# Kernel optimization log

Hardware: AMD Instinct MI355X
Metric: run time of the kernel (lower is better)

Reference implementation:

```python
import jax, jax.numpy as jnp
import numpy as np

B, CIN, COUT, K, E, H, W = 32, 128, 256, 3, 8, 64, 64


def setup_inputs() -> dict:
    key = jax.random.key(0)
    k1, k2, k3, k4 = jax.random.split(key, 4)
    x = jax.random.normal(k1, (B, CIN, H, W), dtype=jnp.float32)
    expert_weight = jax.random.normal(k2, (E, COUT, CIN, K, K), dtype=jnp.float32)
    # nn.Linear(in_channels, num_experts): weight [E, CIN], bias [E]
    bound = 1.0 / np.sqrt(CIN)
    routing_w = jax.random.uniform(k3, (E, CIN), minval=-bound, maxval=bound, dtype=jnp.float32)
    routing_b = jax.random.uniform(k4, (E,), minval=-bound, maxval=bound, dtype=jnp.float32)
    return {"x": x, "expert_weight": expert_weight, "routing_w": routing_w, "routing_b": routing_b}


def reference(x, expert_weight, routing_w, routing_b):
    # routing: global-avg-pool -> linear -> softmax over experts
    pooled = x.mean(axis=(2, 3))                             # [B, CIN]
    logits = pooled @ routing_w.T + routing_b                # [B, E]
    rweights = jax.nn.softmax(logits, axis=-1)               # [B, E]
    # per-sample combined conv weights: [B, COUT, CIN, K, K]
    cw = jnp.einsum('be,eoikl->boikl', rweights, expert_weight)

    def conv_one(xi, wi):
        # xi: [CIN, H, W], wi: [COUT, CIN, K, K]; VALID conv, stride 1
        return jax.lax.conv_general_dilated(
            xi[None], wi, window_strides=(1, 1), padding='VALID',
            dimension_numbers=('NCHW', 'OIHW', 'NCHW'))[0]

    return jax.vmap(conv_one)(x, cw)                         # [B, COUT, H-K+1, W-K+1]
```

## Files before the change

### kernel.cpp

```cpp
#include <hip/hip_runtime.h>
#include <hip/hip_bf16.h>


#define CC_B    32
#define CC_CIN  128
#define CC_COUT 256
#define CC_NP   3844
#define CC_NT   18

typedef __attribute__((ext_vector_type(8))) short bf16x8;
typedef __attribute__((ext_vector_type(4))) float f32x4;

__global__ void cc_nhwc(const float* __restrict__ x, __hip_bfloat16* __restrict__ xn,
                        float* __restrict__ psum) {
    const int b = blockIdx.x >> 6, y = blockIdx.x & 63;
    __shared__ float lds[64 * 129];
    __shared__ float sred[256];
    const int t = threadIdx.x;
    const float* src = x + (size_t)b * CC_CIN * 4096 + y * 64;
#pragma unroll
    for (int i = 0; i < 32; ++i) {
        const int idx = i * 256 + t;
        const int cin = idx >> 6, xx = idx & 63;
        lds[xx * 129 + cin] = src[(size_t)cin * 4096 + xx];
    }
    __syncthreads();
    __hip_bfloat16* dst = xn + ((size_t)b * 4096 + y * 64) * CC_CIN;
#pragma unroll
    for (int j = 0; j < 4; ++j) {
        const int cidx = j * 256 + t;
        const int xx = cidx >> 4, c8 = (cidx & 15) * 8;
        union { __hip_bfloat16 h[8]; uint4 v; } u;
#pragma unroll
        for (int jj = 0; jj < 8; ++jj) u.h[jj] = __float2bfloat16(lds[xx * 129 + c8 + jj]);
        *reinterpret_cast<uint4*>(dst + (size_t)xx * CC_CIN + c8) = u.v;
    }
    const int cin = t & 127, xh = (t >> 7) * 32;
    float s = 0.f;
#pragma unroll
    for (int xx = 0; xx < 32; ++xx) s += lds[(xh + xx) * 129 + cin];
    sred[t] = s;
    __syncthreads();
    if (t < 128) psum[((size_t)b * 64 + y) * CC_CIN + t] = sred[t] + sred[t + 128];
}

__global__ void cc_route(const float* __restrict__ psum,
                         const float* __restrict__ rw_w,
                         const float* __restrict__ rw_b,
                         float* __restrict__ rweights) {
    const int b = blockIdx.x, c = threadIdx.x;
    __shared__ float pl[128];
    __shared__ float lg[8];
    const float* p = psum + (size_t)b * 64 * CC_CIN + c;
    float s = 0.f;
#pragma unroll 8
    for (int y = 0; y < 64; ++y) s += p[(size_t)y * CC_CIN];
    pl[c] = s * (1.f / 4096.f);
    __syncthreads();
    if (c < 8) {
        const float* w = rw_w + c * CC_CIN;
        float a = rw_b[c];
#pragma unroll 8
        for (int i = 0; i < CC_CIN; ++i) a += pl[i] * w[i];
        lg[c] = a;
    }
    __syncthreads();
    if (c == 0) {
        float m = lg[0];
#pragma unroll
        for (int e = 1; e < 8; ++e) m = fmaxf(m, lg[e]);
        float ex[8], sm = 0.f;
#pragma unroll
        for (int e = 0; e < 8; ++e) { ex[e] = __expf(lg[e] - m); sm += ex[e]; }
#pragma unroll
        for (int e = 0; e < 8; ++e) rweights[b * 8 + e] = ex[e] / sm;
    }
}

__global__ void cc_combine(const float* __restrict__ ew,
                           const float* __restrict__ rw,
                           __hip_bfloat16* __restrict__ cw) {
    const int t9 = blockIdx.x >> 8;
    const int cout = blockIdx.x & 255;
    const int cin = threadIdx.x;
    __shared__ float rws[256];
    rws[cin] = rw[cin];
    rws[cin + 128] = rw[cin + 128];
    __syncthreads();
    float wv[8];
    const size_t base = ((size_t)cout * CC_CIN + cin) * 9 + t9;
#pragma unroll
    for (int e = 0; e < 8; ++e) wv[e] = ew[base + (size_t)e * (CC_COUT * CC_CIN * 9)];
#pragma unroll 4
    for (int b = 0; b < CC_B; ++b) {
        float acc = 0.f;
#pragma unroll
        for (int e = 0; e < 8; ++e) acc += rws[b * 8 + e] * wv[e];
        cw[(((size_t)b * 9 + t9) * CC_COUT + cout) * CC_CIN + cin] = __float2bfloat16(acc);
    }
}

__device__ __forceinline__ void gload_lds16(const void* g, void* l) {
    __builtin_amdgcn_global_load_lds(
        (const __attribute__((address_space(1))) unsigned int*)g,
        (__attribute__((address_space(3))) unsigned int*)l, 16, 0, 0);
}

__global__ __launch_bounds__(256, 2) void cc_conv(
    const __hip_bfloat16* __restrict__ xn,
    const __hip_bfloat16* __restrict__ cw,
    float* __restrict__ out)
{
    __shared__ __align__(16) char smem[73728];
    const int l   = blockIdx.x;
    const int xcd = l & 7, li = l >> 3;
    const int b   = 4 * xcd + li / 42;
    const int r2  = li % 42;
    const int nt  = r2 >> 1, mt = r2 & 1;
    const int m0  = mt * 128;
    const int n0  = nt * 186;
    const int y0  = 3 * nt;

    const int tid = threadIdx.x;
    const int wid = tid >> 6, lane = tid & 63;
    const int waveM = wid >> 1, waveN = wid & 1;

    f32x4 acc[4][6];
#pragma unroll
    for (int i = 0; i < 4; ++i)
#pragma unroll
        for (int j = 0; j < 6; ++j) acc[i][j] = (f32x4){0.f, 0.f, 0.f, 0.f};

    const int gsw = (lane & 7) ^ (lane >> 3);
    const __hip_bfloat16* cwb = cw + (size_t)b * 9 * CC_COUT * CC_CIN;
    const __hip_bfloat16* xnb = xn + (size_t)b * 4096 * CC_CIN;

    int laOff[4];
#pragma unroll
    for (int i = 0; i < 4; ++i) {
        const int row = wid * 32 + i * 8 + (lane >> 3);
        laOff[i] = (m0 + row) * CC_CIN + gsw * 8;
    }
    auto stageA = [&](int t) {
        const int h = t / 9, t9 = t - 9 * h;
        const int aoff = t9 * (CC_COUT * CC_CIN) + h * 64;
        char* Ab = smem + (t & 1) * 16384 + wid * 4096;
#pragma unroll
        for (int i = 0; i < 4; ++i)
            gload_lds16(cwb + aoff + laOff[i], Ab + i * 1024);
    };

    char* Bres = smem + 32768;
    auto stageB = [&](int h) {
#pragma unroll
        for (int i = 0; i < 10; ++i) {
            const int row = i * 32 + wid * 8 + (lane >> 3);
            const int yy = row >> 6, x = row & 63;
            int yin = y0 + yy; if (yin > 63) yin = 63;
            gload_lds16(xnb + ((size_t)yin * 64 + x) * CC_CIN + h * 64 + gsw * 8,
                        Bres + i * 4096 + wid * 1024);
        }
    };

    const int rl = lane & 15, q = lane >> 4;

    int pixB[6];
#pragma unroll
    for (int nf = 0; nf < 6; ++nf) {
        int c = waveN * 96 + nf * 16 + rl;
        if (c > 185) c = 185;
        int p = n0 + c; if (p > CC_NP - 1) p = CC_NP - 1;
        const int oy = p / 62;
        pixB[nf] = (oy - y0) * 64 + (p - 62 * oy);
    }

    stageB(0);
    stageA(0);
    stageA(1);

#pragma unroll
    for (int t = 0; t < CC_NT; ++t) {
        const int h = t / 9, t9 = t - 9 * h;
        const int kyx = (t9 / 3) * 64 + (t9 - 3 * (t9 / 3));
        const char* Ab = smem + (t & 1) * 16384;

        if (t < CC_NT - 1) asm volatile("s_waitcnt vmcnt(4)" ::: "memory");
        else               asm volatile("s_waitcnt vmcnt(0)" ::: "memory");
        asm volatile("s_barrier" ::: "memory");

        bf16x8 af[8], bf[12];
#pragma unroll
        for (int mf = 0; mf < 4; ++mf) {
            const int r = waveM * 64 + mf * 16 + rl;
            const char* ap = Ab + r * 128;
            af[mf * 2 + 0] = *(const bf16x8*)(ap + (((q) ^ (r & 7)) * 16));
            af[mf * 2 + 1] = *(const bf16x8*)(ap + (((4 + q) ^ (r & 7)) * 16));
        }
#pragma unroll
        for (int nf = 0; nf < 6; ++nf) {
            const int row = pixB[nf] + kyx;
            const char* bp = Bres + row * 128;
            bf[nf * 2 + 0] = *(const bf16x8*)(bp + (((q) ^ (row & 7)) * 16));
            bf[nf * 2 + 1] = *(const bf16x8*)(bp + (((4 + q) ^ (row & 7)) * 16));
        }
        __builtin_amdgcn_s_setprio(1);
#pragma unroll
        for (int kk = 0; kk < 2; ++kk)
#pragma unroll
            for (int mf = 0; mf < 4; ++mf)
#pragma unroll
                for (int nf = 0; nf < 6; ++nf)
                    acc[mf][nf] = __builtin_amdgcn_mfma_f32_16x16x32_bf16(
                        af[mf * 2 + kk], bf[nf * 2 + kk], acc[mf][nf], 0, 0, 0);
        __builtin_amdgcn_s_setprio(0);

        asm volatile("s_waitcnt lgkmcnt(0)" ::: "memory");
        asm volatile("s_barrier" ::: "memory");
        if (t == 8) stageB(1);
        if (t + 2 < CC_NT) stageA(t + 2);
    }

    const int q4 = (lane >> 4) * 4;
#pragma unroll
    for (int mf = 0; mf < 4; ++mf) {
        const int crow = m0 + waveM * 64 + mf * 16 + q4;
#pragma unroll
        for (int nf = 0; nf < 6; ++nf) {
            const int c = waveN * 96 + nf * 16 + (lane & 15);
            const int p = n0 + c;
            if (c < 186 && p < CC_NP) {
                const size_t ob = ((size_t)b * CC_COUT + crow) * CC_NP + p;
#pragma unroll
                for (int j = 0; j < 4; ++j) out[ob + (size_t)j * CC_NP] = acc[mf][nf][j];
            }
        }
    }
}

extern "C" void kernel_launch(void* const* d_in, const int* in_sizes, int n_in,
                              void* d_out, int out_size, void* d_ws, size_t ws_size,
                              hipStream_t stream) {
    const float* x   = (const float*)d_in[0];
    const float* ew  = (const float*)d_in[1];
    const float* rww = (const float*)d_in[2];
    const float* rwb = (const float*)d_in[3];
    float* out = (float*)d_out;
    char* ws = (char*)d_ws;

    __hip_bfloat16* xnhwc = (__hip_bfloat16*)ws;
    __hip_bfloat16* cwcmb = (__hip_bfloat16*)(ws + 33554432);
    float* psum   = (float*)(ws + 52428800);
    float* rwts   = (float*)(ws + 53493760);

    cc_nhwc<<<dim3(CC_B * 64), dim3(256), 0, stream>>>(x, xnhwc, psum);
    cc_route<<<dim3(CC_B), dim3(128), 0, stream>>>(psum, rww, rwb, rwts);
    cc_combine<<<dim3(9 * CC_COUT), dim3(128), 0, stream>>>(ew, rwts, cwcmb);
    cc_conv<<<dim3(1344), dim3(256), 0, stream>>>(xnhwc, cwcmb, out);
}
```

Baseline: 141.2 us.

## Switch conv GEMM to 32x32x16 MFMA with two-row pixel tiles

The implicit-GEMM conv now uses 32x32x16 bf16 MFMA instructions in place of 16x16x32, with 2x2 fragments per wave. Each block covers 2 output rows (124 pixels) instead of 3 rows (186 pixels), which removes padding waste and the clamping logic and raises the grid from 1344 to 1984 blocks. The larger MFMA is meant to cut LDS fragment reads per FLOP, and the smaller tile is meant to improve load balance. In exchange, the B tile reuse per block drops, and the occupancy hint of 2 blocks per CU is removed from the launch bounds.

```diff
diff --git a/kernel.cpp b/kernel.cpp
--- a/kernel.cpp
+++ b/kernel.cpp
@@ -9,7 +9,7 @@
 #define CC_NT   18
 
 typedef __attribute__((ext_vector_type(8))) short bf16x8;
-typedef __attribute__((ext_vector_type(4))) float f32x4;
+typedef __attribute__((ext_vector_type(16))) float f32x16;
 
 __global__ void cc_nhwc(const float* __restrict__ x, __hip_bfloat16* __restrict__ xn,
                         float* __restrict__ psum) {
@@ -106,30 +106,32 @@
         (__attribute__((address_space(3))) unsigned int*)l, 16, 0, 0);
 }
 
-__global__ __launch_bounds__(256, 2) void cc_conv(
+__global__ __launch_bounds__(256) void cc_conv(
     const __hip_bfloat16* __restrict__ xn,
     const __hip_bfloat16* __restrict__ cw,
     float* __restrict__ out)
 {
-    __shared__ __align__(16) char smem[73728];
+    __shared__ __align__(16) char smem[65536];
     const int l   = blockIdx.x;
     const int xcd = l & 7, li = l >> 3;
-    const int b   = 4 * xcd + li / 42;
-    const int r2  = li % 42;
+    const int b   = 4 * xcd + li / 62;
+    const int r2  = li % 62;
     const int nt  = r2 >> 1, mt = r2 & 1;
     const int m0  = mt * 128;
-    const int n0  = nt * 186;
-    const int y0  = 3 * nt;
+    const int n0  = nt * 124;
+    const int y0  = 2 * nt;
 
     const int tid = threadIdx.x;
     const int wid = tid >> 6, lane = tid & 63;
     const int waveM = wid >> 1, waveN = wid & 1;
 
-    f32x4 acc[4][6];
-#pragma unroll
-    for (int i = 0; i < 4; ++i)
-#pragma unroll
-        for (int j = 0; j < 6; ++j) acc[i][j] = (f32x4){0.f, 0.f, 0.f, 0.f};
+    f32x16 acc[2][2];
+#pragma unroll
+    for (int i = 0; i < 2; ++i)
+#pragma unroll
+        for (int j = 0; j < 2; ++j)
+#pragma unroll
+            for (int v = 0; v < 16; ++v) acc[i][j][v] = 0.f;
 
     const int gsw = (lane & 7) ^ (lane >> 3);
     const __hip_bfloat16* cwb = cw + (size_t)b * 9 * CC_COUT * CC_CIN;
@@ -153,25 +155,22 @@
     char* Bres = smem + 32768;
     auto stageB = [&](int h) {
 #pragma unroll
-        for (int i = 0; i < 10; ++i) {
+        for (int i = 0; i < 8; ++i) {
             const int row = i * 32 + wid * 8 + (lane >> 3);
             const int yy = row >> 6, x = row & 63;
-            int yin = y0 + yy; if (yin > 63) yin = 63;
-            gload_lds16(xnb + ((size_t)yin * 64 + x) * CC_CIN + h * 64 + gsw * 8,
+            gload_lds16(xnb + ((size_t)(y0 + yy) * 64 + x) * CC_CIN + h * 64 + gsw * 8,
                         Bres + i * 4096 + wid * 1024);
         }
     };
 
-    const int rl = lane & 15, q = lane >> 4;
-
-    int pixB[6];
-#pragma unroll
-    for (int nf = 0; nf < 6; ++nf) {
-        int c = waveN * 96 + nf * 16 + rl;
-        if (c > 185) c = 185;
-        int p = n0 + c; if (p > CC_NP - 1) p = CC_NP - 1;
-        const int oy = p / 62;
-        pixB[nf] = (oy - y0) * 64 + (p - 62 * oy);
+    const int l31 = lane & 31, q2 = lane >> 5;
+
+    int pixB[2];
+#pragma unroll
+    for (int nf = 0; nf < 2; ++nf) {
+        int c = nf * 32 + l31;
+        if (c > 61) c = 61;
+        pixB[nf] = waveN * 64 + c;
     }
 
     stageB(0);
@@ -188,30 +187,29 @@
         else               asm volatile("s_waitcnt vmcnt(0)" ::: "memory");
         asm volatile("s_barrier" ::: "memory");
 
-        bf16x8 af[8], bf[12];
-#pragma unroll
-        for (int mf = 0; mf < 4; ++mf) {
-            const int r = waveM * 64 + mf * 16 + rl;
-            const char* ap = Ab + r * 128;
-            af[mf * 2 + 0] = *(const bf16x8*)(ap + (((q) ^ (r & 7)) * 16));
-            af[mf * 2 + 1] = *(const bf16x8*)(ap + (((4 + q) ^ (r & 7)) * 16));
-        }
-#pragma unroll
-        for (int nf = 0; nf < 6; ++nf) {
-            const int row = pixB[nf] + kyx;
-            const char* bp = Bres + row * 128;
-            bf[nf * 2 + 0] = *(const bf16x8*)(bp + (((q) ^ (row & 7)) * 16));
-            bf[nf * 2 + 1] = *(const bf16x8*)(bp + (((4 + q) ^ (row & 7)) * 16));
+        bf16x8 af[2][4], bf[2][4];
+#pragma unroll
+        for (int ks = 0; ks < 4; ++ks) {
+#pragma unroll
+            for (int mf = 0; mf < 2; ++mf) {
+                const int r = waveM * 64 + mf * 32 + l31;
+                af[mf][ks] = *(const bf16x8*)(Ab + r * 128 + (((ks * 2 + q2) ^ (r & 7)) * 16));
+            }
+#pragma unroll
+            for (int nf = 0; nf < 2; ++nf) {
+                const int row = pixB[nf] + kyx;
+                bf[nf][ks] = *(const bf16x8*)(Bres + row * 128 + (((ks * 2 + q2) ^ (row & 7)) * 16));
+            }
         }
         __builtin_amdgcn_s_setprio(1);
 #pragma unroll
-        for (int kk = 0; kk < 2; ++kk)
-#pragma unroll
-            for (int mf = 0; mf < 4; ++mf)
-#pragma unroll
-                for (int nf = 0; nf < 6; ++nf)
-                    acc[mf][nf] = __builtin_amdgcn_mfma_f32_16x16x32_bf16(
-                        af[mf * 2 + kk], bf[nf * 2 + kk], acc[mf][nf], 0, 0, 0);
+        for (int ks = 0; ks < 4; ++ks)
+#pragma unroll
+            for (int mf = 0; mf < 2; ++mf)
+#pragma unroll
+                for (int nf = 0; nf < 2; ++nf)
+                    acc[mf][nf] = __builtin_amdgcn_mfma_f32_32x32x16_bf16(
+                        af[mf][ks], bf[nf][ks], acc[mf][nf], 0, 0, 0);
         __builtin_amdgcn_s_setprio(0);
 
         asm volatile("s_waitcnt lgkmcnt(0)" ::: "memory");
@@ -220,18 +218,21 @@
         if (t + 2 < CC_NT) stageA(t + 2);
     }
 
-    const int q4 = (lane >> 4) * 4;
-#pragma unroll
-    for (int mf = 0; mf < 4; ++mf) {
-        const int crow = m0 + waveM * 64 + mf * 16 + q4;
-#pragma unroll
-        for (int nf = 0; nf < 6; ++nf) {
-            const int c = waveN * 96 + nf * 16 + (lane & 15);
-            const int p = n0 + c;
-            if (c < 186 && p < CC_NP) {
-                const size_t ob = ((size_t)b * CC_COUT + crow) * CC_NP + p;
-#pragma unroll
-                for (int j = 0; j < 4; ++j) out[ob + (size_t)j * CC_NP] = acc[mf][nf][j];
+#pragma unroll
+    for (int mf = 0; mf < 2; ++mf) {
+#pragma unroll
+        for (int nf = 0; nf < 2; ++nf) {
+            const int c2 = nf * 32 + l31;
+            if (c2 < 62) {
+                const int p = n0 + waveN * 62 + c2;
+#pragma unroll
+                for (int g = 0; g < 4; ++g) {
+                    const int crow = m0 + waveM * 64 + mf * 32 + g * 8 + q2 * 4;
+                    const size_t ob = ((size_t)b * CC_COUT + crow) * CC_NP + p;
+#pragma unroll
+                    for (int j = 0; j < 4; ++j)
+                        out[ob + (size_t)j * CC_NP] = acc[mf][nf][g * 4 + j];
+                }
             }
         }
     }
@@ -255,5 +256,5 @@
     cc_nhwc<<<dim3(CC_B * 64), dim3(256), 0, stream>>>(x, xnhwc, psum);
     cc_route<<<dim3(CC_B), dim3(128), 0, stream>>>(psum, rww, rwb, rwts);
     cc_combine<<<dim3(9 * CC_COUT), dim3(128), 0, stream>>>(ew, rwts, cwcmb);
-    cc_conv<<<dim3(1344), dim3(256), 0, stream>>>(xnhwc, cwcmb, out);
-}
+    cc_conv<<<dim3(1984), dim3(256), 0, stream>>>(xnhwc, cwcmb, out);
+}
```

Result: faster. 122.0 us (-13.5%).
